# Optimization experiments

Hardware: AMD Instinct MI355X
Metric: run time of the kernel (lower is better)

Reference implementation:

```python
import jax, jax.numpy as jnp
import numpy as np
import math

FACTOR = 5

def setup_inputs() -> dict:
    key = jax.random.key(0)
    k1, k2, k3 = jax.random.split(key, 3)
    B, L, H, D = 16, 4096, 8, 64
    queries = jax.random.normal(k1, (B, L, H, D), dtype=jnp.float32)
    keys = jax.random.normal(k2, (B, L, H, D), dtype=jnp.float32)
    values = jax.random.normal(k3, (B, L, H, D), dtype=jnp.float32)
    # Periodic sampling indices, mirroring _periorprob_QK's loop over outputFFT
    # (synthetic periods; index_K = L_K - (i+1)*P for each period P <= L_K)
    L_K = L
    sample_k = min(FACTOR * math.ceil(math.log(L_K)), L_K)  # U_part = 45
    periods = [24, 96, 168]
    idx = []
    for p in periods:
        for i in range(math.ceil(L_K / p)):
            v = L_K - (i + 1) * p
            if v >= 0:
                idx.append(v)
    index_k = jnp.asarray(np.array(idx[:sample_k], dtype=np.int32))
    return {"queries": queries, "keys": keys, "values": values, "index_k": index_k}


def reference(queries, keys, values, index_k):
    B, L_Q, H, D = queries.shape
    L_K = keys.shape[1]
    u = min(FACTOR * math.ceil(math.log(L_Q)), L_Q)  # n_top
    scale = 1.0 / math.sqrt(D)

    Q = jnp.transpose(queries, (0, 2, 1, 3))  # [B,H,L_Q,D]
    K = jnp.transpose(keys, (0, 2, 1, 3))     # [B,H,L_K,D]
    V = jnp.transpose(values, (0, 2, 1, 3))   # [B,H,L_V,D]

    # K_sample_amp_K = K_sample * K_sample (K_sample_amp is overwritten by K_sample
    # in the original); sampled rows are the same for every query position.
    K2 = K[:, :, index_k, :] ** 2                              # [B,H,S,D]
    Q_K_sample = jnp.einsum('bhqd,bhsd->bhqs', Q, K2)          # [B,H,L_Q,S]
    M = Q_K_sample.max(-1) - Q_K_sample.sum(-1) / L_K          # sparsity measure
    _, M_top = jax.lax.top_k(M, u)                             # [B,H,u]

    Q_reduce = jnp.take_along_axis(Q, M_top[..., None], axis=2)  # [B,H,u,D]
    scores = jnp.einsum('bhud,bhkd->bhuk', Q_reduce, K) * scale  # [B,H,u,L_K]

    # ProbMask: causal mask on the selected query rows
    key_pos = jnp.arange(L_K)
    mask = key_pos[None, None, None, :] > M_top[..., None]
    scores = jnp.where(mask, -jnp.inf, scores)
    attn = jax.nn.softmax(scores, axis=-1)
    ctx_update = jnp.einsum('bhuk,bhkd->bhud', attn, V)        # [B,H,u,D]

    # initial context = cumsum of V (mask_flag=True branch), scatter top queries
    context = jnp.cumsum(V, axis=2)                            # [B,H,L_Q,D]
    b_idx = jnp.arange(B)[:, None, None]
    h_idx = jnp.arange(H)[None, :, None]
    context = context.at[b_idx, h_idx, M_top].set(ctx_update)
    return jnp.transpose(context, (0, 2, 1, 3))                # [B,L_Q,H,D]
```

## Files before the change

### kernel.cpp

```cpp
#include <hip/hip_runtime.h>
#include <math.h>

#define B_ 16
#define L_ 4096
#define H_ 8
#define D_ 64
#define HD_ (H_*D_)
#define U_ 45
#define UP_ 48
#define NCHUNK 32
#define CHLEN 128
#define QP 68

__device__ inline float blo(unsigned int u) { return __uint_as_float(u << 16); }
__device__ inline float bhi(unsigned int u) { return __uint_as_float(u & 0xFFFF0000u); }
__device__ inline unsigned int pk2(float a, float b) {
    return (__float_as_uint(b) & 0xFFFF0000u) | (__float_as_uint(a) >> 16);
}

__global__ __launch_bounds__(256) void kM(const float* __restrict__ Q, const float* __restrict__ K,
                                          const int* __restrict__ idx, int S, float* __restrict__ M) {
    int blk = blockIdx.x;
    int chunk = blk & 15;
    int bh = blk >> 4;
    int b = bh >> 3, h = bh & 7;
    __shared__ float k2[45 * 64];
    for (int i = threadIdx.x; i < S * D_; i += 256) {
        int s = i >> 6, d = i & 63;
        float kv = K[(((size_t)b * L_ + idx[s]) * H_ + h) * D_ + d];
        k2[i] = kv * kv;
    }
    __syncthreads();
    int q = chunk * 256 + threadIdx.x;
    const float4* qp = (const float4*)(Q + (((size_t)b * L_ + q) * H_ + h) * D_);
    float4 qr[16];
#pragma unroll
    for (int c = 0; c < 16; c++) qr[c] = qp[c];
    float mx = -INFINITY, sm = 0.f;
    for (int s = 0; s < S; s++) {
        const float4* kp = (const float4*)(k2 + s * D_);
        float d0 = 0, d1 = 0, d2 = 0, d3 = 0;
#pragma unroll
        for (int c = 0; c < 16; c++) {
            float4 kv = kp[c];
            d0 += qr[c].x * kv.x; d1 += qr[c].y * kv.y;
            d2 += qr[c].z * kv.z; d3 += qr[c].w * kv.w;
        }
        float dot = (d0 + d1) + (d2 + d3);
        mx = fmaxf(mx, dot); sm += dot;
    }
    M[(size_t)bh * L_ + q] = mx - sm * (1.0f / (float)L_);
}

__global__ __launch_bounds__(256) void kTop(const float* __restrict__ M, int* __restrict__ mtop) {
    int bh = blockIdx.x, t = threadIdx.x;
    int lane = t & 63, wid = t >> 6;
    float mv[16];
#pragma unroll
    for (int w = 0; w < 16; w++) mv[w] = M[(size_t)bh * L_ + w * 256 + t];
    __shared__ float swv[4];
    __shared__ int swi[4];
    for (int it = 0; it < U_; it++) {
        float bv = -INFINITY; int bi = 1 << 30;
#pragma unroll
        for (int w = 0; w < 16; w++) {
            if (mv[w] > bv) { bv = mv[w]; bi = w * 256 + t; }
        }
#pragma unroll
        for (int off = 1; off < 64; off <<= 1) {
            float ov = __shfl_xor(bv, off); int oi = __shfl_xor(bi, off);
            if (ov > bv || (ov == bv && oi < bi)) { bv = ov; bi = oi; }
        }
        if (lane == 0) { swv[wid] = bv; swi[wid] = bi; }
        __syncthreads();
        float fv = swv[0]; int fi = swi[0];
        for (int w2 = 1; w2 < 4; w2++) {
            if (swv[w2] > fv || (swv[w2] == fv && swi[w2] < fi)) { fv = swv[w2]; fi = swi[w2]; }
        }
        if (t == 0) mtop[bh * U_ + it] = fi;
        int wr = fi >> 8;
        bool own = ((fi & 255) == t);
#pragma unroll
        for (int w = 0; w < 16; w++) mv[w] = (own && w == wr) ? -INFINITY : mv[w];
        __syncthreads();
    }
}

__global__ __launch_bounds__(64) void kSum(const float* __restrict__ V, float* __restrict__ cs) {
    int blk = blockIdx.x;
    int c = blk & 31, bh = blk >> 5;
    int b = bh >> 3, h = bh & 7;
    size_t base = (((size_t)b * L_ + c * CHLEN) * H_ + h) * D_ + threadIdx.x;
    float acc = 0.f;
#pragma unroll 8
    for (int i = 0; i < CHLEN; i++) acc += V[base + (size_t)i * HD_];
    cs[((size_t)bh * NCHUNK + c) * D_ + threadIdx.x] = acc;
}

__global__ __launch_bounds__(64) void kScan(float* __restrict__ cs) {
    int bh = blockIdx.x;
    int d = threadIdx.x;
    float run = 0.f;
    for (int c = 0; c < NCHUNK; c++) {
        size_t i = ((size_t)bh * NCHUNK + c) * D_ + d;
        float t = cs[i]; cs[i] = run; run += t;
    }
}

__global__ __launch_bounds__(64) void kCum(const float* __restrict__ V, const float* __restrict__ cs,
                                           float* __restrict__ out) {
    int blk = blockIdx.x;
    int c = blk & 31, bh = blk >> 5;
    int b = bh >> 3, h = bh & 7;
    size_t base = (((size_t)b * L_ + c * CHLEN) * H_ + h) * D_ + threadIdx.x;
    float acc = cs[((size_t)bh * NCHUNK + c) * D_ + threadIdx.x];
#pragma unroll 4
    for (int i = 0; i < CHLEN; i++) {
        acc += V[base + (size_t)i * HD_];
        out[base + (size_t)i * HD_] = acc;
    }
}

__global__ __launch_bounds__(128, 2) void kFlash(const float* __restrict__ Q, const float* __restrict__ K,
                                                 const float* __restrict__ V, const int* __restrict__ mtop,
                                                 float* __restrict__ Opart, float* __restrict__ mpart,
                                                 float* __restrict__ lpart, int nsb, int wkspan) {
    int blk = blockIdx.x;
    int ks = blk % nsb;
    int bh = blk / nsb;
    int b = bh >> 3, h = bh & 7;
    int tid = threadIdx.x, wave = tid >> 6, lane = tid & 63;
    int qg = lane >> 3, kg = lane & 7;
    int qg6 = qg * 6;

    __shared__ unsigned short KsT[2][64 * 64];
    __shared__ unsigned short Vs[2][64 * 64];
    __shared__ unsigned short Qs[UP_ * QP];
    __shared__ int mt[UP_];
    __shared__ int kmaxs;

    if (tid < UP_) mt[tid] = (tid < U_) ? mtop[bh * U_ + tid] : -1;
    __syncthreads();
    if (tid == 0) {
        int km = 0;
        for (int u = 0; u < U_; u++) km = max(km, mt[u] + 1);
        kmaxs = km;
    }
    for (int i = tid; i < UP_ * 16; i += 128) {
        int q = i >> 4, cc = i & 15;
        int r = mt[q] < 0 ? 0 : mt[q];
        const float4 qv = *(const float4*)(Q + (((size_t)b * L_ + r) * H_ + h) * D_ + cc * 4);
        *(uint2*)(Qs + q * QP + cc * 4) =
            make_uint2(pk2(qv.x * 0.125f, qv.y * 0.125f), pk2(qv.z * 0.125f, qv.w * 0.125f));
    }
    __syncthreads();

    int mtr[6];
#pragma unroll
    for (int qq = 0; qq < 6; qq++) mtr[qq] = mt[qg6 + qq];

    float o[6][8];
#pragma unroll
    for (int qq = 0; qq < 6; qq++)
#pragma unroll
        for (int dd = 0; dd < 8; dd++) o[qq][dd] = 0.f;
    float mrow[6], lrow[6];
#pragma unroll
    for (int qq = 0; qq < 6; qq++) { mrow[qq] = -INFINITY; lrow[qq] = 0.f; }

    int ko = (ks * 2 + wave) * wkspan;
    int kend = min(kmaxs, ko + wkspan);

    for (int jt = ko; jt < kend; jt += 64) {
        for (int i = lane; i < 64 * 16; i += 64) {
            int r = i >> 4, cc = i & 15;
            size_t g = (((size_t)b * L_ + jt + r) * H_ + h) * D_ + cc * 4;
            const float4 kv = *(const float4*)(K + g);
            const float4 vv = *(const float4*)(V + g);
            *(uint2*)(Vs[wave] + r * 64 + cc * 4) = make_uint2(pk2(vv.x, vv.y), pk2(vv.z, vv.w));
            int g8 = r >> 3, kk = r & 7;
            int sw = (cc & 7);
            float kx[4] = { kv.x, kv.y, kv.z, kv.w };
#pragma unroll
            for (int t2 = 0; t2 < 4; t2++) {
                int d = cc * 4 + t2;
                KsT[wave][d * 64 + (((g8 ^ sw) << 3) | kk)] =
                    (unsigned short)(__float_as_uint(kx[t2]) >> 16);
            }
        }
        float s[6][8];
#pragma unroll
        for (int qq = 0; qq < 6; qq++)
#pragma unroll
            for (int kk = 0; kk < 8; kk++) s[qq][kk] = 0.f;
        for (int ch = 0; ch < 16; ch++) {
            float qv[6][4];
#pragma unroll
            for (int qq = 0; qq < 6; qq++) {
                const uint2 u = *(const uint2*)(Qs + (qg6 + qq) * QP + ch * 4);
                qv[qq][0] = blo(u.x); qv[qq][1] = bhi(u.x);
                qv[qq][2] = blo(u.y); qv[qq][3] = bhi(u.y);
            }
            const int koff = (kg ^ (ch & 7)) << 3;
#pragma unroll
            for (int dd = 0; dd < 4; dd++) {
                const uint4 u = *(const uint4*)(KsT[wave] + (ch * 4 + dd) * 64 + koff);
                float kv[8] = { blo(u.x), bhi(u.x), blo(u.y), bhi(u.y),
                                blo(u.z), bhi(u.z), blo(u.w), bhi(u.w) };
#pragma unroll
                for (int qq = 0; qq < 6; qq++)
#pragma unroll
                    for (int kk = 0; kk < 8; kk++)
                        s[qq][kk] = fmaf(qv[qq][dd], kv[kk], s[qq][kk]);
            }
        }
        int colb = jt + kg * 8;
        float al[6];
#pragma unroll
        for (int qq = 0; qq < 6; qq++) {
            float tm = -INFINITY;
#pragma unroll
            for (int kk = 0; kk < 8; kk++)
                if (colb + kk <= mtr[qq]) tm = fmaxf(tm, s[qq][kk]);
            tm = fmaxf(tm, __shfl_xor(tm, 1));
            tm = fmaxf(tm, __shfl_xor(tm, 2));
            tm = fmaxf(tm, __shfl_xor(tm, 4));
            float nm = fmaxf(mrow[qq], tm);
            float a = (nm == -INFINITY) ? 1.f : __expf(mrow[qq] - nm);
            mrow[qq] = nm;
            float rs = 0.f;
#pragma unroll
            for (int kk = 0; kk < 8; kk++) {
                float p = (colb + kk <= mtr[qq]) ? __expf(s[qq][kk] - nm) : 0.f;
                s[qq][kk] = p; rs += p;
            }
            rs += __shfl_xor(rs, 1);
            rs += __shfl_xor(rs, 2);
            rs += __shfl_xor(rs, 4);
            lrow[qq] = lrow[qq] * a + rs;
            al[qq] = a;
        }
#pragma unroll
        for (int qq = 0; qq < 6; qq++)
#pragma unroll
            for (int dd = 0; dd < 8; dd++) o[qq][dd] *= al[qq];
        unsigned int ps[3][8];
#pragma unroll
        for (int pp = 0; pp < 3; pp++)
#pragma unroll
            for (int kk = 0; kk < 8; kk++) ps[pp][kk] = pk2(s[2 * pp][kk], s[2 * pp + 1][kk]);
        for (int jg = 0; jg < 8; jg++) {
            const int srcaddr = ((lane & 56) | jg) << 2;
#pragma unroll
            for (int jj = 0; jj < 8; jj++) {
                const int j = jg * 8 + jj;
                int p01 = __builtin_amdgcn_ds_bpermute(srcaddr, (int)ps[0][jj]);
                int p23 = __builtin_amdgcn_ds_bpermute(srcaddr, (int)ps[1][jj]);
                int p45 = __builtin_amdgcn_ds_bpermute(srcaddr, (int)ps[2][jj]);
                const uint4 u = *(const uint4*)(Vs[wave] + j * 64 + kg * 8);
                float vv[8] = { blo(u.x), bhi(u.x), blo(u.y), bhi(u.y),
                                blo(u.z), bhi(u.z), blo(u.w), bhi(u.w) };
                float pq[6] = { blo((unsigned)p01), bhi((unsigned)p01),
                                blo((unsigned)p23), bhi((unsigned)p23),
                                blo((unsigned)p45), bhi((unsigned)p45) };
#pragma unroll
                for (int qq = 0; qq < 6; qq++)
#pragma unroll
                    for (int dd = 0; dd < 8; dd++)
                        o[qq][dd] = fmaf(pq[qq], vv[dd], o[qq][dd]);
            }
        }
    }
    int nse = nsb * 2;
    int e = ks * 2 + wave;
    float* ob = Opart + ((size_t)(bh * nse + e)) * UP_ * D_;
#pragma unroll
    for (int qq = 0; qq < 6; qq++) {
        int q = qg6 + qq;
        *(float4*)(ob + q * D_ + kg * 8) = make_float4(o[qq][0], o[qq][1], o[qq][2], o[qq][3]);
        *(float4*)(ob + q * D_ + kg * 8 + 4) = make_float4(o[qq][4], o[qq][5], o[qq][6], o[qq][7]);
    }
    if (kg == 0) {
#pragma unroll
        for (int qq = 0; qq < 6; qq++) {
            mpart[(size_t)(bh * nse + e) * UP_ + qg6 + qq] = mrow[qq];
            lpart[(size_t)(bh * nse + e) * UP_ + qg6 + qq] = lrow[qq];
        }
    }
}

__global__ __launch_bounds__(256) void kMerge(const float* __restrict__ Opart, const float* __restrict__ mpart,
                                              const float* __restrict__ lpart, const int* __restrict__ mtop,
                                              float* __restrict__ out, int nse) {
    int bh = blockIdx.x; int b = bh >> 3, h = bh & 7;
    for (int idx = threadIdx.x; idx < U_ * D_; idx += 256) {
        int q = idx >> 6, d = idx & 63;
        float mmax = -INFINITY;
        for (int i = 0; i < nse; i++) mmax = fmaxf(mmax, mpart[(size_t)(bh * nse + i) * UP_ + q]);
        float Ls = 0.f, val = 0.f;
        for (int i = 0; i < nse; i++) {
            float w = __expf(mpart[(size_t)(bh * nse + i) * UP_ + q] - mmax);
            Ls += lpart[(size_t)(bh * nse + i) * UP_ + q] * w;
            val += Opart[((size_t)(bh * nse + i) * UP_ + q) * D_ + d] * w;
        }
        int m = mtop[bh * U_ + q];
        out[(((size_t)b * L_ + m) * H_ + h) * D_ + d] = val / Ls;
    }
}

extern "C" void kernel_launch(void* const* d_in, const int* in_sizes, int n_in,
                              void* d_out, int out_size, void* d_ws, size_t ws_size,
                              hipStream_t stream) {
    const float* Q = (const float*)d_in[0];
    const float* K = (const float*)d_in[1];
    const float* V = (const float*)d_in[2];
    const int* idx = (const int*)d_in[3];
    int S = in_sizes[3]; if (S > 45) S = 45;
    float* out = (float*)d_out;
    float* ws = (float*)d_ws;

    size_t wsf = ws_size / 4;
    int nsb = 8;
    while (nsb > 1) {
        size_t opart = (size_t)128 * (2 * nsb) * UP_ * D_;
        size_t need = 5760 + opart + 2 * (size_t)128 * (2 * nsb) * UP_;
        size_t needAB = 5760 + 524288 + 262144;
        if (need <= wsf && needAB <= wsf) break;
        nsb >>= 1;
    }
    int nse = 2 * nsb;

    int* mtop = (int*)ws;
    float* rest = ws + 5760;
    float* M = rest;
    float* cs = rest + 524288;
    float* Opart = rest;
    float* mpart = Opart + (size_t)128 * nse * UP_ * D_;
    float* lpart = mpart + (size_t)128 * nse * UP_;

    kM   <<<B_ * H_ * (L_ / 256), 256, 0, stream>>>(Q, K, idx, S, M);
    kTop <<<B_ * H_,              256, 0, stream>>>(M, mtop);
    kSum <<<B_ * H_ * NCHUNK,      64, 0, stream>>>(V, cs);
    kScan<<<B_ * H_,               64, 0, stream>>>(cs);
    kCum <<<B_ * H_ * NCHUNK,      64, 0, stream>>>(V, cs, out);
    kFlash<<<B_ * H_ * nsb,       128, 0, stream>>>(Q, K, V, mtop, Opart, mpart, lpart, nsb, L_ / nse);
    kMerge<<<B_ * H_,             256, 0, stream>>>(Opart, mpart, lpart, mtop, out, nse);
}
```

Before: 703.5 us.

## Use bf16 MFMA for flash attention and precompute squared sampled keys

Rewrites the sparse attention kernel to compute QK^T and PV with bf16 16x16x32 MFMA instructions instead of scalar FMA on bf16-unpacked values. K fragments now load straight from global memory into registers, and V and P are staged transposed in small LDS tiles. Key tiles shrink to 32 rows and the split count doubles. The squared sampled-key computation moves into its own kernel so the M kernel reads it from global memory rather than rebuilding it per block. This adds a kernel launch and extra workspace, and relies on the MFMA fragment layouts being correct.

```diff
diff --git a/kernel.cpp b/kernel.cpp
--- a/kernel.cpp
+++ b/kernel.cpp
@@ -10,35 +10,45 @@
 #define UP_ 48
 #define NCHUNK 32
 #define CHLEN 128
-#define QP 68
-
-__device__ inline float blo(unsigned int u) { return __uint_as_float(u << 16); }
-__device__ inline float bhi(unsigned int u) { return __uint_as_float(u & 0xFFFF0000u); }
+#define VTP 20
+#define PP  20
+
+typedef __attribute__((ext_vector_type(8))) short short8v;
+typedef __attribute__((ext_vector_type(4))) float f32x4;
+
 __device__ inline unsigned int pk2(float a, float b) {
     return (__float_as_uint(b) & 0xFFFF0000u) | (__float_as_uint(a) >> 16);
 }
-
-__global__ __launch_bounds__(256) void kM(const float* __restrict__ Q, const float* __restrict__ K,
-                                          const int* __restrict__ idx, int S, float* __restrict__ M) {
+__device__ inline short8v u4cast(uint4 u) {
+    union { uint4 u4; short8v s8; } c; c.u4 = u; return c.s8;
+}
+
+__global__ __launch_bounds__(256) void kK2(const float* __restrict__ K, const int* __restrict__ idx,
+                                           int S, float* __restrict__ k2) {
+    int bh = blockIdx.x;
+    int b = bh >> 3, h = bh & 7;
+    for (int i = threadIdx.x; i < S * D_; i += 256) {
+        int s = i >> 6, d = i & 63;
+        float kv = K[(((size_t)b * L_ + idx[s]) * H_ + h) * D_ + d];
+        k2[(size_t)bh * (45 * 64) + i] = kv * kv;
+    }
+}
+
+__global__ __launch_bounds__(256) void kM(const float* __restrict__ Q, const float* __restrict__ k2g,
+                                          int S, float* __restrict__ M) {
     int blk = blockIdx.x;
     int chunk = blk & 15;
     int bh = blk >> 4;
     int b = bh >> 3, h = bh & 7;
-    __shared__ float k2[45 * 64];
-    for (int i = threadIdx.x; i < S * D_; i += 256) {
-        int s = i >> 6, d = i & 63;
-        float kv = K[(((size_t)b * L_ + idx[s]) * H_ + h) * D_ + d];
-        k2[i] = kv * kv;
-    }
-    __syncthreads();
     int q = chunk * 256 + threadIdx.x;
     const float4* qp = (const float4*)(Q + (((size_t)b * L_ + q) * H_ + h) * D_);
     float4 qr[16];
 #pragma unroll
     for (int c = 0; c < 16; c++) qr[c] = qp[c];
+    const float4* kp0 = (const float4*)(k2g + (size_t)bh * (45 * 64));
     float mx = -INFINITY, sm = 0.f;
     for (int s = 0; s < S; s++) {
-        const float4* kp = (const float4*)(k2 + s * D_);
+        const float4* kp = kp0 + s * 16;
         float d0 = 0, d1 = 0, d2 = 0, d3 = 0;
 #pragma unroll
         for (int c = 0; c < 16; c++) {
@@ -121,23 +131,24 @@
     }
 }
 
-__global__ __launch_bounds__(128, 2) void kFlash(const float* __restrict__ Q, const float* __restrict__ K,
-                                                 const float* __restrict__ V, const int* __restrict__ mtop,
-                                                 float* __restrict__ Opart, float* __restrict__ mpart,
-                                                 float* __restrict__ lpart, int nsb, int wkspan) {
+__global__ __launch_bounds__(128) void kFlash(const float* __restrict__ Q, const float* __restrict__ K,
+                                              const float* __restrict__ V, const int* __restrict__ mtop,
+                                              float* __restrict__ Opart, float* __restrict__ mpart,
+                                              float* __restrict__ lpart, int nsb, int wkspan) {
     int blk = blockIdx.x;
     int ks = blk % nsb;
     int bh = blk / nsb;
     int b = bh >> 3, h = bh & 7;
     int tid = threadIdx.x, wave = tid >> 6, lane = tid & 63;
-    int qg = lane >> 3, kg = lane & 7;
-    int qg6 = qg * 6;
-
-    __shared__ unsigned short KsT[2][64 * 64];
-    __shared__ unsigned short Vs[2][64 * 64];
-    __shared__ unsigned short Qs[UP_ * QP];
+    int q16 = lane & 15, g = lane >> 4;
+
+    __shared__ __align__(16) unsigned int VtS[2][64 * VTP];
+    __shared__ __align__(16) unsigned int PS[2][UP_ * PP];
     __shared__ int mt[UP_];
     __shared__ int kmaxs;
+
+    unsigned int* Vt = VtS[wave];
+    unsigned int* P = PS[wave];
 
     if (tid < UP_) mt[tid] = (tid < U_) ? mtop[bh * U_ + tid] : -1;
     __syncthreads();
@@ -146,145 +157,162 @@
         for (int u = 0; u < U_; u++) km = max(km, mt[u] + 1);
         kmaxs = km;
     }
-    for (int i = tid; i < UP_ * 16; i += 128) {
-        int q = i >> 4, cc = i & 15;
-        int r = mt[q] < 0 ? 0 : mt[q];
-        const float4 qv = *(const float4*)(Q + (((size_t)b * L_ + r) * H_ + h) * D_ + cc * 4);
-        *(uint2*)(Qs + q * QP + cc * 4) =
-            make_uint2(pk2(qv.x * 0.125f, qv.y * 0.125f), pk2(qv.z * 0.125f, qv.w * 0.125f));
+
+    int mtr[3];
+    short8v qf[3][2];
+#pragma unroll
+    for (int t = 0; t < 3; t++) {
+        int qi = t * 16 + q16;
+        mtr[t] = mt[qi];
+        int r = mtr[t] < 0 ? 0 : mtr[t];
+        const float* qrow = Q + (((size_t)b * L_ + r) * H_ + h) * D_;
+#pragma unroll
+        for (int s = 0; s < 2; s++) {
+            int d0 = s * 32 + g * 8;
+            float4 f0 = *(const float4*)(qrow + d0);
+            float4 f1 = *(const float4*)(qrow + d0 + 4);
+            uint4 u;
+            u.x = pk2(f0.x * 0.125f, f0.y * 0.125f);
+            u.y = pk2(f0.z * 0.125f, f0.w * 0.125f);
+            u.z = pk2(f1.x * 0.125f, f1.y * 0.125f);
+            u.w = pk2(f1.z * 0.125f, f1.w * 0.125f);
+            qf[t][s] = u4cast(u);
+        }
     }
     __syncthreads();
 
-    int mtr[6];
-#pragma unroll
-    for (int qq = 0; qq < 6; qq++) mtr[qq] = mt[qg6 + qq];
-
-    float o[6][8];
-#pragma unroll
-    for (int qq = 0; qq < 6; qq++)
-#pragma unroll
-        for (int dd = 0; dd < 8; dd++) o[qq][dd] = 0.f;
-    float mrow[6], lrow[6];
-#pragma unroll
-    for (int qq = 0; qq < 6; qq++) { mrow[qq] = -INFINITY; lrow[qq] = 0.f; }
+    f32x4 Oa[4][3];
+#pragma unroll
+    for (int dt = 0; dt < 4; dt++)
+#pragma unroll
+        for (int t = 0; t < 3; t++) Oa[dt][t] = (f32x4){0.f, 0.f, 0.f, 0.f};
+    float mrow[3] = {-INFINITY, -INFINITY, -INFINITY};
+    float lrow[3] = {0.f, 0.f, 0.f};
 
     int ko = (ks * 2 + wave) * wkspan;
     int kend = min(kmaxs, ko + wkspan);
 
-    for (int jt = ko; jt < kend; jt += 64) {
-        for (int i = lane; i < 64 * 16; i += 64) {
-            int r = i >> 4, cc = i & 15;
-            size_t g = (((size_t)b * L_ + jt + r) * H_ + h) * D_ + cc * 4;
-            const float4 kv = *(const float4*)(K + g);
-            const float4 vv = *(const float4*)(V + g);
-            *(uint2*)(Vs[wave] + r * 64 + cc * 4) = make_uint2(pk2(vv.x, vv.y), pk2(vv.z, vv.w));
-            int g8 = r >> 3, kk = r & 7;
-            int sw = (cc & 7);
-            float kx[4] = { kv.x, kv.y, kv.z, kv.w };
-#pragma unroll
-            for (int t2 = 0; t2 < 4; t2++) {
-                int d = cc * 4 + t2;
-                KsT[wave][d * 64 + (((g8 ^ sw) << 3) | kk)] =
-                    (unsigned short)(__float_as_uint(kx[t2]) >> 16);
+    for (int jt = ko; jt < kend; jt += 32) {
+        const float* vrow0 = V + (((size_t)b * L_ + jt + 2 * q16) * H_ + h) * D_;
+        const float* vrow1 = vrow0 + HD_;
+        float4 va[4], vb[4];
+#pragma unroll
+        for (int i = 0; i < 4; i++) {
+            int d0 = i * 16 + g * 4;
+            va[i] = *(const float4*)(vrow0 + d0);
+            vb[i] = *(const float4*)(vrow1 + d0);
+        }
+        f32x4 Sa[3][2];
+#pragma unroll
+        for (int t = 0; t < 3; t++)
+#pragma unroll
+            for (int n = 0; n < 2; n++) Sa[t][n] = (f32x4){0.f, 0.f, 0.f, 0.f};
+#pragma unroll
+        for (int s = 0; s < 2; s++) {
+            short8v kf[2];
+#pragma unroll
+            for (int n = 0; n < 2; n++) {
+                const float* krow = K + (((size_t)b * L_ + jt + n * 16 + q16) * H_ + h) * D_ + s * 32 + g * 8;
+                float4 f0 = *(const float4*)krow;
+                float4 f1 = *(const float4*)(krow + 4);
+                uint4 u;
+                u.x = pk2(f0.x, f0.y); u.y = pk2(f0.z, f0.w);
+                u.z = pk2(f1.x, f1.y); u.w = pk2(f1.z, f1.w);
+                kf[n] = u4cast(u);
             }
-        }
-        float s[6][8];
-#pragma unroll
-        for (int qq = 0; qq < 6; qq++)
-#pragma unroll
-            for (int kk = 0; kk < 8; kk++) s[qq][kk] = 0.f;
-        for (int ch = 0; ch < 16; ch++) {
-            float qv[6][4];
-#pragma unroll
-            for (int qq = 0; qq < 6; qq++) {
-                const uint2 u = *(const uint2*)(Qs + (qg6 + qq) * QP + ch * 4);
-                qv[qq][0] = blo(u.x); qv[qq][1] = bhi(u.x);
-                qv[qq][2] = blo(u.y); qv[qq][3] = bhi(u.y);
+#pragma unroll
+            for (int t = 0; t < 3; t++)
+#pragma unroll
+                for (int n = 0; n < 2; n++)
+                    Sa[t][n] = __builtin_amdgcn_mfma_f32_16x16x32_bf16(kf[n], qf[t][s], Sa[t][n], 0, 0, 0);
+        }
+#pragma unroll
+        for (int t = 0; t < 3; t++) {
+            int limit = mtr[t];
+            int kb = jt + g * 4;
+            float p[2][4];
+            float pmax = -INFINITY;
+#pragma unroll
+            for (int n = 0; n < 2; n++)
+#pragma unroll
+                for (int r = 0; r < 4; r++) {
+                    float sv = (kb + n * 16 + r <= limit) ? Sa[t][n][r] : -INFINITY;
+                    p[n][r] = sv;
+                    pmax = fmaxf(pmax, sv);
+                }
+            pmax = fmaxf(pmax, __shfl_xor(pmax, 16));
+            pmax = fmaxf(pmax, __shfl_xor(pmax, 32));
+            float nm = fmaxf(mrow[t], pmax);
+            float alpha = (nm == -INFINITY) ? 1.f : __expf(mrow[t] - nm);
+            mrow[t] = nm;
+            float rs = 0.f;
+#pragma unroll
+            for (int n = 0; n < 2; n++)
+#pragma unroll
+                for (int r = 0; r < 4; r++) {
+                    float pv = (p[n][r] == -INFINITY) ? 0.f : __expf(p[n][r] - nm);
+                    p[n][r] = pv; rs += pv;
+                }
+            rs += __shfl_xor(rs, 16);
+            rs += __shfl_xor(rs, 32);
+            lrow[t] = lrow[t] * alpha + rs;
+            int qi = t * 16 + q16;
+#pragma unroll
+            for (int n = 0; n < 2; n++) {
+                *(uint2*)&P[qi * PP + n * 8 + 2 * g] =
+                    make_uint2(pk2(p[n][0], p[n][1]), pk2(p[n][2], p[n][3]));
             }
-            const int koff = (kg ^ (ch & 7)) << 3;
-#pragma unroll
-            for (int dd = 0; dd < 4; dd++) {
-                const uint4 u = *(const uint4*)(KsT[wave] + (ch * 4 + dd) * 64 + koff);
-                float kv[8] = { blo(u.x), bhi(u.x), blo(u.y), bhi(u.y),
-                                blo(u.z), bhi(u.z), blo(u.w), bhi(u.w) };
-#pragma unroll
-                for (int qq = 0; qq < 6; qq++)
-#pragma unroll
-                    for (int kk = 0; kk < 8; kk++)
-                        s[qq][kk] = fmaf(qv[qq][dd], kv[kk], s[qq][kk]);
+#pragma unroll
+            for (int dt = 0; dt < 4; dt++)
+#pragma unroll
+                for (int r = 0; r < 4; r++) Oa[dt][t][r] *= alpha;
+        }
+#pragma unroll
+        for (int i = 0; i < 4; i++) {
+            int d0 = i * 16 + g * 4;
+#pragma unroll
+            for (int c = 0; c < 4; c++) {
+                float fa = (&va[i].x)[c], fb = (&vb[i].x)[c];
+                Vt[(d0 + c) * VTP + q16] = pk2(fa, fb);
             }
         }
-        int colb = jt + kg * 8;
-        float al[6];
-#pragma unroll
-        for (int qq = 0; qq < 6; qq++) {
-            float tm = -INFINITY;
-#pragma unroll
-            for (int kk = 0; kk < 8; kk++)
-                if (colb + kk <= mtr[qq]) tm = fmaxf(tm, s[qq][kk]);
-            tm = fmaxf(tm, __shfl_xor(tm, 1));
-            tm = fmaxf(tm, __shfl_xor(tm, 2));
-            tm = fmaxf(tm, __shfl_xor(tm, 4));
-            float nm = fmaxf(mrow[qq], tm);
-            float a = (nm == -INFINITY) ? 1.f : __expf(mrow[qq] - nm);
-            mrow[qq] = nm;
-            float rs = 0.f;
-#pragma unroll
-            for (int kk = 0; kk < 8; kk++) {
-                float p = (colb + kk <= mtr[qq]) ? __expf(s[qq][kk] - nm) : 0.f;
-                s[qq][kk] = p; rs += p;
-            }
-            rs += __shfl_xor(rs, 1);
-            rs += __shfl_xor(rs, 2);
-            rs += __shfl_xor(rs, 4);
-            lrow[qq] = lrow[qq] * a + rs;
-            al[qq] = a;
-        }
-#pragma unroll
-        for (int qq = 0; qq < 6; qq++)
-#pragma unroll
-            for (int dd = 0; dd < 8; dd++) o[qq][dd] *= al[qq];
-        unsigned int ps[3][8];
-#pragma unroll
-        for (int pp = 0; pp < 3; pp++)
-#pragma unroll
-            for (int kk = 0; kk < 8; kk++) ps[pp][kk] = pk2(s[2 * pp][kk], s[2 * pp + 1][kk]);
-        for (int jg = 0; jg < 8; jg++) {
-            const int srcaddr = ((lane & 56) | jg) << 2;
-#pragma unroll
-            for (int jj = 0; jj < 8; jj++) {
-                const int j = jg * 8 + jj;
-                int p01 = __builtin_amdgcn_ds_bpermute(srcaddr, (int)ps[0][jj]);
-                int p23 = __builtin_amdgcn_ds_bpermute(srcaddr, (int)ps[1][jj]);
-                int p45 = __builtin_amdgcn_ds_bpermute(srcaddr, (int)ps[2][jj]);
-                const uint4 u = *(const uint4*)(Vs[wave] + j * 64 + kg * 8);
-                float vv[8] = { blo(u.x), bhi(u.x), blo(u.y), bhi(u.y),
-                                blo(u.z), bhi(u.z), blo(u.w), bhi(u.w) };
-                float pq[6] = { blo((unsigned)p01), bhi((unsigned)p01),
-                                blo((unsigned)p23), bhi((unsigned)p23),
-                                blo((unsigned)p45), bhi((unsigned)p45) };
-#pragma unroll
-                for (int qq = 0; qq < 6; qq++)
-#pragma unroll
-                    for (int dd = 0; dd < 8; dd++)
-                        o[qq][dd] = fmaf(pq[qq], vv[dd], o[qq][dd]);
-            }
-        }
-    }
+        short8v pb[3];
+#pragma unroll
+        for (int t = 0; t < 3; t++)
+            pb[t] = u4cast(*(uint4*)&P[(t * 16 + q16) * PP + g * 4]);
+#pragma unroll
+        for (int dt = 0; dt < 4; dt++) {
+            short8v vf = u4cast(*(uint4*)&Vt[(dt * 16 + q16) * VTP + g * 4]);
+#pragma unroll
+            for (int t = 0; t < 3; t++)
+                Oa[dt][t] = __builtin_amdgcn_mfma_f32_16x16x32_bf16(vf, pb[t], Oa[dt][t], 0, 0, 0);
+        }
+    }
+
     int nse = nsb * 2;
     int e = ks * 2 + wave;
     float* ob = Opart + ((size_t)(bh * nse + e)) * UP_ * D_;
-#pragma unroll
-    for (int qq = 0; qq < 6; qq++) {
-        int q = qg6 + qq;
-        *(float4*)(ob + q * D_ + kg * 8) = make_float4(o[qq][0], o[qq][1], o[qq][2], o[qq][3]);
-        *(float4*)(ob + q * D_ + kg * 8 + 4) = make_float4(o[qq][4], o[qq][5], o[qq][6], o[qq][7]);
-    }
-    if (kg == 0) {
-#pragma unroll
-        for (int qq = 0; qq < 6; qq++) {
-            mpart[(size_t)(bh * nse + e) * UP_ + qg6 + qq] = mrow[qq];
-            lpart[(size_t)(bh * nse + e) * UP_ + qg6 + qq] = lrow[qq];
+    int q2 = lane >> 2, c2 = lane & 3;
+#pragma unroll
+    for (int t = 0; t < 3; t++) {
+#pragma unroll
+        for (int dt = 0; dt < 4; dt++) {
+            f32x4 o = Oa[dt][t];
+            *(uint4*)&Vt[q16 * 68 + dt * 16 + g * 4] =
+                make_uint4(__float_as_uint(o[0]), __float_as_uint(o[1]),
+                           __float_as_uint(o[2]), __float_as_uint(o[3]));
+        }
+#pragma unroll
+        for (int j = 0; j < 4; j++) {
+            uint4 u = *(uint4*)&Vt[q2 * 68 + j * 16 + c2 * 4];
+            *(float4*)(ob + (size_t)(t * 16 + q2) * D_ + j * 16 + c2 * 4) =
+                make_float4(__uint_as_float(u.x), __uint_as_float(u.y),
+                            __uint_as_float(u.z), __uint_as_float(u.w));
+        }
+        if (g == 0) {
+            int qi = t * 16 + q16;
+            mpart[(size_t)(bh * nse + e) * UP_ + qi] = mrow[t];
+            lpart[(size_t)(bh * nse + e) * UP_ + qi] = lrow[t];
         }
     }
 }
@@ -320,11 +348,11 @@
     float* ws = (float*)d_ws;
 
     size_t wsf = ws_size / 4;
-    int nsb = 8;
+    int nsb = 16;
     while (nsb > 1) {
         size_t opart = (size_t)128 * (2 * nsb) * UP_ * D_;
         size_t need = 5760 + opart + 2 * (size_t)128 * (2 * nsb) * UP_;
-        size_t needAB = 5760 + 524288 + 262144;
+        size_t needAB = 5760 + 524288 + 262144 + 368640;
         if (need <= wsf && needAB <= wsf) break;
         nsb >>= 1;
     }
@@ -334,11 +362,13 @@
     float* rest = ws + 5760;
     float* M = rest;
     float* cs = rest + 524288;
+    float* k2 = rest + 524288 + 262144;
     float* Opart = rest;
     float* mpart = Opart + (size_t)128 * nse * UP_ * D_;
     float* lpart = mpart + (size_t)128 * nse * UP_;
 
-    kM   <<<B_ * H_ * (L_ / 256), 256, 0, stream>>>(Q, K, idx, S, M);
+    kK2  <<<B_ * H_,              256, 0, stream>>>(K, idx, S, k2);
+    kM   <<<B_ * H_ * (L_ / 256), 256, 0, stream>>>(Q, k2, S, M);
     kTop <<<B_ * H_,              256, 0, stream>>>(M, mtop);
     kSum <<<B_ * H_ * NCHUNK,      64, 0, stream>>>(V, cs);
     kScan<<<B_ * H_,               64, 0, stream>>>(cs);
```

Result: slower. 734.4 us (+4.4%).
